# Performance work log

Measured on AMD Instinct MI355X. Metric: run time of the kernel, lower is better.

The kernel has to match this reference:

```python
import jax, jax.numpy as jnp
import numpy as np

EPS = 1e-5  # torch LayerNorm default


def _ln(x, g, b):
    mu = jnp.mean(x, axis=-1, keepdims=True)
    var = jnp.var(x, axis=-1, keepdims=True)
    return (x - mu) * jax.lax.rsqrt(var + EPS) * g + b


def _linear(x, w, b):
    # torch nn.Linear: y = x @ W^T + b, W is [out, in]
    return jnp.einsum('bnc,dc->bnd', x, w) + b


def setup_inputs() -> dict:
    key = jax.random.key(0)
    ks = jax.random.split(key, 12)
    B, C, H, W = 16, 768, 32, 32
    s = 1.0 / np.sqrt(C)
    inp = {
        'x_rgb': jax.random.normal(ks[0], (B, C, H, W), jnp.float32),
        'x_tir': jax.random.normal(ks[1], (B, C, H, W), jnp.float32),
        'x_before': jax.random.normal(ks[2], (B, C, H, W), jnp.float32),
        'w0': jax.random.uniform(ks[3], (C, C), jnp.float32, -s, s),
        'b0': jax.random.uniform(ks[4], (C,), jnp.float32, -s, s),
        'w1': jax.random.uniform(ks[5], (C, C), jnp.float32, -s, s),
        'b1': jax.random.uniform(ks[6], (C,), jnp.float32, -s, s),
        'w2': jax.random.uniform(ks[7], (C, C), jnp.float32, -s, s),
        'b2': jax.random.uniform(ks[8], (C,), jnp.float32, -s, s),
        'ln_g': jnp.ones((C,), jnp.float32),
        'ln_b': jnp.zeros((C,), jnp.float32),
        'wp': jax.random.uniform(ks[9], (C, C), jnp.float32, -s, s),
        'bp': jax.random.uniform(ks[10], (C,), jnp.float32, -s, s),
    }
    return inp


def reference(x_rgb, x_tir, x_before, w0, b0, w1, b1, w2, b2, ln_g, ln_b, wp, bp):
    B, C, H, W = x_rgb.shape
    N = H * W
    scale = C ** (-0.5)
    # flatten(2).permute(0,2,1): [B,C,H,W] -> [B, N, C]
    to_tok = lambda x: jnp.transpose(x.reshape(B, C, N), (0, 2, 1))
    r = _linear(_ln(to_tok(x_rgb), ln_g, ln_b), w0, b0)
    t = _linear(_ln(to_tok(x_tir), ln_g, ln_b), w1, b1)
    f = _linear(_ln(to_tok(x_before), ln_g, ln_b), w2, b2)
    x_sum = r + t
    x_mul = r * t
    # attention: [B, N, N]
    attn = jax.nn.softmax(jnp.einsum('bnc,bmc->bnm', r, f) * scale, axis=-1)
    mid = jnp.einsum('bnm,bmc->bnc', attn, t)
    # faithful to torch: .transpose(1,2).reshape(B, N, C) (element reorder)
    mid = jnp.transpose(mid, (0, 2, 1)).reshape(B, N, C)
    x_middle = x_sum + mid
    x_middle = x_middle + _linear(_ln(x_middle, ln_g, ln_b), wp, bp)
    res = jax.nn.gelu(x_sum, approximate=False) * x_middle \
        + jax.nn.gelu(x_mul, approximate=False) * x_middle
    return res.reshape(B, C, H, W)
```

## Files before the change

### kernel.cpp

```cpp
#include <hip/hip_runtime.h>
#include <hip/hip_bf16.h>
#include <math.h>

typedef unsigned short u16;
typedef __attribute__((ext_vector_type(8))) short bf16x8;
typedef __attribute__((ext_vector_type(4))) float f32x4;
typedef __attribute__((ext_vector_type(4))) u16 u16x4;

#define DEVI static __device__ __forceinline__

DEVI float bf2f(u16 h){ union{unsigned u; float f;} v; v.u=((unsigned)h)<<16; return v.f; }
DEVI u16 f2bf(float x){ union{float f; unsigned u;} v; v.f=x; unsigned r=v.u+0x7fffu+((v.u>>16)&1u); return (u16)(r>>16); }
DEVI void split2(float x, u16 &h, u16 &l){ h=f2bf(x); l=f2bf(x-bf2f(h)); }
DEVI float geluf(float x){ return 0.5f*x*(1.0f+erff(x*0.70710678118654752f)); }

#define GLD16(g,s) __builtin_amdgcn_global_load_lds((const __attribute__((address_space(1))) void*)(g), (__attribute__((address_space(3))) void*)(s), 16, 0, 0)

__global__ void ln_stats_k(const float* __restrict__ x0, const float* __restrict__ x1,
                           const float* __restrict__ x2, float* __restrict__ muS,
                           float* __restrict__ rsS)
{
  const int inp = blockIdx.y;
  const float* x = inp==0?x0:(inp==1?x1:x2);
  const int T0 = blockIdx.x*64;
  const int b = T0>>10, n0 = T0&1023;
  const int tid = threadIdx.x;
  const int n = tid&63, part = tid>>6;
  const float* base = x + ((size_t)b*768)*1024 + n0 + n;
  float s=0.f, s2=0.f;
  for (int c=part;c<768;c+=4){ float v = base[(size_t)c*1024]; s+=v; s2+=v*v; }
  __shared__ float r1[256], r2[256];
  r1[tid]=s; r2[tid]=s2; __syncthreads();
  if (tid<64){
    s = r1[tid]+r1[tid+64]+r1[tid+128]+r1[tid+192];
    s2= r2[tid]+r2[tid+64]+r2[tid+128]+r2[tid+192];
    float mu = s*(1.f/768.f);
    float var = s2*(1.f/768.f)-mu*mu;
    muS[inp*16384+T0+tid]=mu;
    rsS[inp*16384+T0+tid]=rsqrtf(var+1e-5f);
  }
}

__global__ void ln_apply_k(const float* __restrict__ x, const float* __restrict__ muS,
                           const float* __restrict__ rsS, const float* __restrict__ g,
                           const float* __restrict__ be, u16* __restrict__ Ah,
                           u16* __restrict__ Al, int inp)
{
  const int b = blockIdx.y;
  const int gx = blockIdx.x;
  const int c0=(gx%24)*32, n0=(gx/24)*32;
  const int tid=threadIdx.x;
  __shared__ u16 Hh[32][33], Hl[32][33];
  const int nl=tid&31, cp=tid>>5;
  const int tok = b*1024 + n0 + nl;
  const float mu = muS[inp*16384+tok], rs = rsS[inp*16384+tok];
  #pragma unroll
  for (int i=0;i<4;i++){
    int cl = cp + i*8;
    int c = c0 + cl;
    float v = x[((size_t)(b*768+c))*1024 + n0 + nl];
    float y = (v-mu)*rs*g[c]+be[c];
    u16 h,l; split2(y,h,l);
    Hh[cl][nl]=h; Hl[cl][nl]=l;
  }
  __syncthreads();
  const int wn = tid>>3, wc=(tid&7)*4;
  u16x4 vh, vl;
  #pragma unroll
  for (int j=0;j<4;j++){ vh[j]=Hh[wc+j][wn]; vl[j]=Hl[wc+j][wn]; }
  size_t o = ((size_t)(b*1024+n0+wn))*768 + c0 + wc;
  *(u16x4*)(Ah+o)=vh; *(u16x4*)(Al+o)=vl;
}

__global__ void wsplit_k(const float* __restrict__ w0,const float* __restrict__ w1,
                         const float* __restrict__ w2,const float* __restrict__ wpk,
                         u16* __restrict__ wh, u16* __restrict__ wl)
{
  const int ws = blockIdx.y;
  const float* w = ws==0?w0:(ws==1?w1:(ws==2?w2:wpk));
  int i = blockIdx.x*256+threadIdx.x;
  u16 h,l; split2(w[i],h,l);
  wh[(size_t)ws*589824+i]=h; wl[(size_t)ws*589824+i]=l;
}

__global__ void tr_pairs_k(const u16* __restrict__ Sh, const u16* __restrict__ Sl,
                           u16* __restrict__ Dh, u16* __restrict__ Dl)
{
  const int b = blockIdx.y;
  const int gx = blockIdx.x;
  const int c0=(gx%24)*32, n0=(gx/24)*32;
  const int tid=threadIdx.x;
  __shared__ u16 Th[32][33], Tl[32][33];
  const int cl=tid&31, np=tid>>5;
  #pragma unroll
  for (int i=0;i<4;i++){
    int nl = np + i*8;
    size_t o = ((size_t)(b*1024+n0+nl))*768 + c0 + cl;
    Th[cl][nl]=Sh[o]; Tl[cl][nl]=Sl[o];
  }
  __syncthreads();
  const int nl2=tid&31, cp2=tid>>5;
  #pragma unroll
  for (int i=0;i<4;i++){
    int cl2 = cp2 + i*8;
    size_t o = ((size_t)b*786432) + (size_t)(c0+cl2)*1024 + n0 + nl2;
    Dh[o]=Th[cl2][nl2]; Dl[o]=Tl[cl2][nl2];
  }
}

__global__ void softmax_k(float* __restrict__ S)
{
  const long row = blockIdx.x;
  const int tid=threadIdx.x;
  const int lane=tid&63, wid=tid>>6;
  float4 v4 = *(const float4*)(S + row*1024 + tid*4);
  float m = fmaxf(fmaxf(v4.x,v4.y),fmaxf(v4.z,v4.w));
  for (int o=1;o<64;o<<=1) m = fmaxf(m, __shfl_xor(m,o,64));
  __shared__ float red[4]; __shared__ float red2[4];
  if (lane==0) red[wid]=m;
  __syncthreads();
  m = fmaxf(fmaxf(red[0],red[1]),fmaxf(red[2],red[3]));
  float e0=__expf(v4.x-m), e1=__expf(v4.y-m), e2=__expf(v4.z-m), e3=__expf(v4.w-m);
  float s = e0+e1+e2+e3;
  for (int o=1;o<64;o<<=1) s += __shfl_xor(s,o,64);
  if (lane==0) red2[wid]=s;
  __syncthreads();
  s = red2[0]+red2[1]+red2[2]+red2[3];
  float inv = 1.f/s;
  u16x4 h4,l4;
  u16 h,l;
  split2(e0*inv,h,l); h4[0]=h; l4[0]=l;
  split2(e1*inv,h,l); h4[1]=h; l4[1]=l;
  split2(e2*inv,h,l); h4[2]=h; l4[2]=l;
  split2(e3*inv,h,l); h4[3]=h; l4[3]=l;
  u16* base = (u16*)S + row*2048;
  *(u16x4*)(base + tid*4)        = h4;
  *(u16x4*)(base + 1024 + tid*4) = l4;
}

__global__ void midtr_k(const float* __restrict__ mid, const u16* __restrict__ rh,
                        const u16* __restrict__ rl, const u16* __restrict__ th,
                        const u16* __restrict__ tl, float* __restrict__ xm)
{
  const int b=blockIdx.y;
  const int gx=blockIdx.x;
  const int c0=(gx%24)*32, n0=(gx/24)*32;
  const int tid=threadIdx.x;
  __shared__ float T[32][33];
  const int cl=tid&31, np=tid>>5;
  #pragma unroll
  for (int i=0;i<4;i++){
    int nl=np+i*8;
    T[cl][nl] = mid[((size_t)b*786432)+(size_t)(n0+nl)*768 + c0+cl];
  }
  __syncthreads();
  const int nl2=tid&31, cp2=tid>>5;
  #pragma unroll
  for (int i=0;i<4;i++){
    int cl2=cp2+i*8;
    size_t j = (size_t)(c0+cl2)*1024 + n0+nl2;
    size_t gi = (size_t)b*786432 + j;
    float rv = bf2f(rh[gi])+bf2f(rl[gi]);
    float tv = bf2f(th[gi])+bf2f(tl[gi]);
    xm[gi] = rv+tv+T[cl2][nl2];
  }
}

__global__ void ln_rows_k(const float* __restrict__ x, const float* __restrict__ g,
                          const float* __restrict__ be, u16* __restrict__ Oh, u16* __restrict__ Ol)
{
  const long row=blockIdx.x;
  const int tid=threadIdx.x;
  const float* xr = x + row*768;
  float v0=xr[tid], v1=xr[tid+256], v2=xr[tid+512];
  float s=v0+v1+v2, s2=v0*v0+v1*v1+v2*v2;
  for (int o=1;o<64;o<<=1){ s+=__shfl_xor(s,o,64); s2+=__shfl_xor(s2,o,64); }
  __shared__ float rA[4]; __shared__ float rB[4];
  const int lane=tid&63, wid=tid>>6;
  if(lane==0){rA[wid]=s;rB[wid]=s2;}
  __syncthreads();
  s=rA[0]+rA[1]+rA[2]+rA[3]; s2=rB[0]+rB[1]+rB[2]+rB[3];
  float mu=s*(1.f/768.f), var=s2*(1.f/768.f)-mu*mu, rs=rsqrtf(var+1e-5f);
  u16 h,l;
  float y0=(v0-mu)*rs*g[tid]+be[tid];         split2(y0,h,l); Oh[row*768+tid]=h;     Ol[row*768+tid]=l;
  float y1=(v1-mu)*rs*g[tid+256]+be[tid+256]; split2(y1,h,l); Oh[row*768+tid+256]=h; Ol[row*768+tid+256]=l;
  float y2=(v2-mu)*rs*g[tid+512]+be[tid+512]; split2(y2,h,l); Oh[row*768+tid+512]=h; Ol[row*768+tid+512]=l;
}

template<int EPI>
__launch_bounds__(256,2)
__global__ void gemm3_k(const u16* __restrict__ Ah, const u16* __restrict__ Al, long aBat, int lda,
                        const u16* __restrict__ Bh, const u16* __restrict__ Bl, long bBat, int ldb,
                        int K, int tilesM, int ldo, long oBat, float scaleV,
                        const float* __restrict__ bias,
                        u16* __restrict__ Oh, u16* __restrict__ Ol,
                        float* __restrict__ outF,
                        const float* __restrict__ xmid,
                        const u16* __restrict__ rhp, const u16* __restrict__ rlp,
                        const u16* __restrict__ thp, const u16* __restrict__ tlp,
                        float* __restrict__ dout)
{
  __shared__ u16 sm[16384];
  u16* sAh=sm; u16* sAl=sm+4096; u16* sBh=sm+8192; u16* sBl=sm+12288;
  const int tid=threadIdx.x, lane=tid&63, wid=tid>>6;
  const int wm=(wid&1)*64, wn=(wid>>1)*64;
  const int tm = (blockIdx.x % tilesM)*128;
  const int tn = (blockIdx.x / tilesM)*128;
  const int batch = blockIdx.y;
  const u16* gAh = Ah + (long)batch*aBat + (long)tm*lda;
  const u16* gAl = Al + (long)batch*aBat + (long)tm*lda;
  const u16* gBh = Bh + (long)batch*bBat + (long)tn*ldb;
  const u16* gBl = Bl + (long)batch*bBat + (long)tn*ldb;
  f32x4 acc[4][4];
  #pragma unroll
  for(int i=0;i<4;i++)
    #pragma unroll
    for(int j=0;j<4;j++) acc[i][j]=(f32x4){0.f,0.f,0.f,0.f};
  const int frow=lane&15, fko=(lane>>4)<<3;
  const int nkt=K>>5;
  for(int kt=0;kt<nkt;kt++){
    const int k0=kt<<5;
    __syncthreads();
    #pragma unroll
    for(int is=0;is<2;is++){
      int idx=is*256+tid;
      int mm=idx>>2, ko=(idx&3)<<3;
      long goA=(long)mm*lda + k0 + ko;
      long goB=(long)mm*ldb + k0 + ko;
      int so=(idx & ~63)*8;
      GLD16(gAh+goA, sAh+so);
      GLD16(gAl+goA, sAl+so);
      GLD16(gBh+goB, sBh+so);
      GLD16(gBl+goB, sBl+so);
    }
    __syncthreads();
    bf16x8 fbh[4], fbl[4];
    #pragma unroll
    for(int j=0;j<4;j++){
      int off=(wn+j*16+frow)*32+fko;
      fbh[j]=*(const bf16x8*)(sBh+off);
      fbl[j]=*(const bf16x8*)(sBl+off);
    }
    #pragma unroll
    for(int i=0;i<4;i++){
      int off=(wm+i*16+frow)*32+fko;
      bf16x8 fah=*(const bf16x8*)(sAh+off);
      bf16x8 fal=*(const bf16x8*)(sAl+off);
      #pragma unroll
      for(int j=0;j<4;j++){
        acc[i][j]=__builtin_amdgcn_mfma_f32_16x16x32_bf16(fah,fbh[j],acc[i][j],0,0,0);
        acc[i][j]=__builtin_amdgcn_mfma_f32_16x16x32_bf16(fah,fbl[j],acc[i][j],0,0,0);
        acc[i][j]=__builtin_amdgcn_mfma_f32_16x16x32_bf16(fal,fbh[j],acc[i][j],0,0,0);
      }
    }
  }
  const int r0 = tm+wm+((lane>>4)<<2);
  const int c0 = tn+wn+(lane&15);
  #pragma unroll
  for(int i=0;i<4;i++){
    #pragma unroll
    for(int q=0;q<4;q++){
      int r = r0 + i*16 + q;
      #pragma unroll
      for(int j=0;j<4;j++){
        int cc = c0 + j*16;
        float v = acc[i][j][q];
        long o = (long)batch*oBat + (long)(r>>10)*oBat + (long)(r&1023)*ldo + cc;
        if constexpr (EPI==0){
          v += bias[cc];
          u16 h,l; split2(v,h,l);
          Oh[o]=h; Ol[o]=l;
        } else if constexpr (EPI==1){
          outF[o] = v*scaleV;
        } else if constexpr (EPI==2){
          outF[o] = v;
        } else {
          float lin = v + bias[cc];
          float xmv = xmid[o];
          float rv = bf2f(rhp[o])+bf2f(rlp[o]);
          float tv = bf2f(thp[o])+bf2f(tlp[o]);
          float xs=rv+tv, xmu=rv*tv;
          dout[o] = (geluf(xs)+geluf(xmu))*(xmv+lin);
        }
      }
    }
  }
}

extern "C" void kernel_launch(void* const* d_in, const int* in_sizes, int n_in,
                              void* d_out, int out_size, void* d_ws, size_t ws_size,
                              hipStream_t stream)
{
  const float* x_rgb=(const float*)d_in[0];
  const float* x_tir=(const float*)d_in[1];
  const float* x_bef=(const float*)d_in[2];
  const float* w0=(const float*)d_in[3];
  const float* b0=(const float*)d_in[4];
  const float* w1=(const float*)d_in[5];
  const float* b1=(const float*)d_in[6];
  const float* w2=(const float*)d_in[7];
  const float* b2=(const float*)d_in[8];
  const float* lng=(const float*)d_in[9];
  const float* lnb=(const float*)d_in[10];
  const float* wpk=(const float*)d_in[11];
  const float* bp=(const float*)d_in[12];
  float* out=(float*)d_out;

  char* wsb=(char*)d_ws;
  size_t off=0;
  auto alloc=[&](size_t bytes)->char*{ char* p=wsb+off; off=(off+bytes+255)&~(size_t)255; return p; };

  const long PAIRE = (long)16384*768;
  float* muS = (float*)alloc(3*16384*4);
  float* rsS = (float*)alloc(3*16384*4);
  u16* wh = (u16*)alloc(4*589824*2);
  u16* wl = (u16*)alloc(4*589824*2);
  char* stageA = alloc((size_t)2*PAIRE*2);
  u16* sAh=(u16*)stageA;      u16* sAl=sAh+PAIRE;
  u16* tTh=sAh;               u16* tTl=sAh+PAIRE;
  u16* xmh=sAh;               u16* xml=sAh+PAIRE;
  u16* rh=(u16*)alloc(PAIRE*2); u16* rl=(u16*)alloc(PAIRE*2);
  u16* th=(u16*)alloc(PAIRE*2); u16* tl=(u16*)alloc(PAIRE*2);
  char* fmid = alloc((size_t)2*PAIRE*2);
  u16* fb=(u16*)fmid;
  float* midf=(float*)fmid;
  char* SPx = alloc((size_t)2*PAIRE*2);
  float* Sf=(float*)SPx;
  u16* Pu=(u16*)SPx;
  float* xmf=(float*)SPx;

  if (off > ws_size){
    hipMemsetAsync(d_out, 0, (size_t)out_size*4, stream);
    return;
  }

  const float SC = 0.03608439182435161f;
  dim3 blk(256);

  wsplit_k<<<dim3(2304,4),blk,0,stream>>>(w0,w1,w2,wpk,wh,wl);
  ln_stats_k<<<dim3(256,3),blk,0,stream>>>(x_rgb,x_tir,x_bef,muS,rsS);

  ln_apply_k<<<dim3(768,16),blk,0,stream>>>(x_rgb,muS,rsS,lng,lnb,sAh,sAl,0);
  gemm3_k<0><<<dim3(128*6,1),blk,0,stream>>>(sAh,sAl,0,768, wh,wl,0,768, 768,128,768,786432, 0.f,
      b0, rh,rl, nullptr, nullptr,nullptr,nullptr,nullptr,nullptr,nullptr);
  ln_apply_k<<<dim3(768,16),blk,0,stream>>>(x_tir,muS,rsS,lng,lnb,sAh,sAl,1);
  gemm3_k<0><<<dim3(128*6,1),blk,0,stream>>>(sAh,sAl,0,768, wh+589824,wl+589824,0,768, 768,128,768,786432, 0.f,
      b1, th,tl, nullptr, nullptr,nullptr,nullptr,nullptr,nullptr,nullptr);
  ln_apply_k<<<dim3(768,16),blk,0,stream>>>(x_bef,muS,rsS,lng,lnb,sAh,sAl,2);
  gemm3_k<0><<<dim3(128*6,1),blk,0,stream>>>(sAh,sAl,0,768, wh+2*589824,wl+2*589824,0,768, 768,128,768,1572864, 0.f,
      b2, fb,fb+786432, nullptr, nullptr,nullptr,nullptr,nullptr,nullptr,nullptr);

  tr_pairs_k<<<dim3(768,16),blk,0,stream>>>(th,tl,tTh,tTl);

  for (int c=0;c<2;c++){
    long cb = (long)c*8;
    gemm3_k<1><<<dim3(8*8,8),blk,0,stream>>>(rh+cb*786432,rl+cb*786432,786432,768,
        fb+cb*1572864,fb+786432+cb*1572864,1572864,768,
        768,8,1024,1048576, SC, nullptr, nullptr,nullptr, Sf,
        nullptr,nullptr,nullptr,nullptr,nullptr,nullptr);
    softmax_k<<<dim3(8192),blk,0,stream>>>(Sf);
    gemm3_k<2><<<dim3(8*6,8),blk,0,stream>>>(Pu,Pu+1024,2097152,2048,
        tTh+cb*786432,tTl+cb*786432,786432,1024,
        1024,8,768,786432, 0.f, nullptr, nullptr,nullptr, midf+cb*786432,
        nullptr,nullptr,nullptr,nullptr,nullptr,nullptr);
  }

  midtr_k<<<dim3(768,16),blk,0,stream>>>(midf,rh,rl,th,tl,xmf);
  ln_rows_k<<<dim3(16384),blk,0,stream>>>(xmf,lng,lnb,xmh,xml);
  gemm3_k<3><<<dim3(128*6,1),blk,0,stream>>>(xmh,xml,0,768, wh+3*589824,wl+3*589824,0,768,
      768,128,768,786432, 0.f, bp, nullptr,nullptr, nullptr, xmf, rh,rl,th,tl, out);
}
```

Baseline: 921.3 us.

## Fuse mid transpose and residual add into PV GEMM epilogue; split LN stats

Adds an EPI==4 epilogue to the attention-times-T GEMM that writes its result transposed and adds r+t directly into x_middle, which removes the separate midtr_k transpose kernel and its extra round trip through global memory. LayerNorm statistics are now computed with a two-stage reduction: a partial-sum kernel with more blocks and float4 loads over channel chunks, then a finalize kernel. This raises parallelism for the stats pass. The transposed stores in the fused epilogue are strided across columns, which may coalesce poorly, and workspace layout changes so midf is reused as x_middle.

```diff
diff --git a/kernel.cpp b/kernel.cpp
--- a/kernel.cpp
+++ b/kernel.cpp
@@ -16,29 +16,45 @@
 
 #define GLD16(g,s) __builtin_amdgcn_global_load_lds((const __attribute__((address_space(1))) void*)(g), (__attribute__((address_space(3))) void*)(s), 16, 0, 0)
 
-__global__ void ln_stats_k(const float* __restrict__ x0, const float* __restrict__ x1,
-                           const float* __restrict__ x2, float* __restrict__ muS,
-                           float* __restrict__ rsS)
+__global__ void ln_part_k(const float* __restrict__ x0, const float* __restrict__ x1,
+                          const float* __restrict__ x2, float* __restrict__ sP,
+                          float* __restrict__ s2P)
 {
   const int inp = blockIdx.y;
   const float* x = inp==0?x0:(inp==1?x1:x2);
-  const int T0 = blockIdx.x*64;
+  const int tile = blockIdx.x>>3, chunk = blockIdx.x&7;
+  const int T0 = tile*256;
   const int b = T0>>10, n0 = T0&1023;
-  const int tid = threadIdx.x;
-  const int n = tid&63, part = tid>>6;
-  const float* base = x + ((size_t)b*768)*1024 + n0 + n;
+  const int tid = threadIdx.x, lane = tid&63, part = tid>>6;
+  const float* base = x + ((size_t)b*768 + chunk*96)*1024 + n0 + lane*4;
+  float4 s = {0,0,0,0}, s2 = {0,0,0,0};
+  for (int c=part; c<96; c+=4){
+    float4 v = *(const float4*)(base + (size_t)c*1024);
+    s.x+=v.x; s.y+=v.y; s.z+=v.z; s.w+=v.w;
+    s2.x+=v.x*v.x; s2.y+=v.y*v.y; s2.z+=v.z*v.z; s2.w+=v.w*v.w;
+  }
+  __shared__ float4 L1[4][64], L2[4][64];
+  L1[part][lane]=s; L2[part][lane]=s2;
+  __syncthreads();
+  const float* f1=(const float*)L1; const float* f2=(const float*)L2;
+  float a  = f1[tid]+f1[256+tid]+f1[512+tid]+f1[768+tid];
+  float a2 = f2[tid]+f2[256+tid]+f2[512+tid]+f2[768+tid];
+  long o = (long)inp*131072 + (long)chunk*16384 + T0 + tid;
+  sP[o]=a; s2P[o]=a2;
+}
+
+__global__ void ln_fin_k(const float* __restrict__ sP, const float* __restrict__ s2P,
+                         float* __restrict__ muS, float* __restrict__ rsS)
+{
+  int i = blockIdx.x*256+threadIdx.x;
+  int inp = i>>14, ti = i&16383;
+  long base = (long)inp*131072 + ti;
   float s=0.f, s2=0.f;
-  for (int c=part;c<768;c+=4){ float v = base[(size_t)c*1024]; s+=v; s2+=v*v; }
-  __shared__ float r1[256], r2[256];
-  r1[tid]=s; r2[tid]=s2; __syncthreads();
-  if (tid<64){
-    s = r1[tid]+r1[tid+64]+r1[tid+128]+r1[tid+192];
-    s2= r2[tid]+r2[tid+64]+r2[tid+128]+r2[tid+192];
-    float mu = s*(1.f/768.f);
-    float var = s2*(1.f/768.f)-mu*mu;
-    muS[inp*16384+T0+tid]=mu;
-    rsS[inp*16384+T0+tid]=rsqrtf(var+1e-5f);
-  }
+  #pragma unroll
+  for (int k=0;k<8;k++){ s += sP[base+(long)k*16384]; s2 += s2P[base+(long)k*16384]; }
+  float mu = s*(1.f/768.f);
+  float var = s2*(1.f/768.f)-mu*mu;
+  muS[i]=mu; rsS[i]=rsqrtf(var+1e-5f);
 }
 
 __global__ void ln_apply_k(const float* __restrict__ x, const float* __restrict__ muS,
@@ -136,34 +152,6 @@
   u16* base = (u16*)S + row*2048;
   *(u16x4*)(base + tid*4)        = h4;
   *(u16x4*)(base + 1024 + tid*4) = l4;
-}
-
-__global__ void midtr_k(const float* __restrict__ mid, const u16* __restrict__ rh,
-                        const u16* __restrict__ rl, const u16* __restrict__ th,
-                        const u16* __restrict__ tl, float* __restrict__ xm)
-{
-  const int b=blockIdx.y;
-  const int gx=blockIdx.x;
-  const int c0=(gx%24)*32, n0=(gx/24)*32;
-  const int tid=threadIdx.x;
-  __shared__ float T[32][33];
-  const int cl=tid&31, np=tid>>5;
-  #pragma unroll
-  for (int i=0;i<4;i++){
-    int nl=np+i*8;
-    T[cl][nl] = mid[((size_t)b*786432)+(size_t)(n0+nl)*768 + c0+cl];
-  }
-  __syncthreads();
-  const int nl2=tid&31, cp2=tid>>5;
-  #pragma unroll
-  for (int i=0;i<4;i++){
-    int cl2=cp2+i*8;
-    size_t j = (size_t)(c0+cl2)*1024 + n0+nl2;
-    size_t gi = (size_t)b*786432 + j;
-    float rv = bf2f(rh[gi])+bf2f(rl[gi]);
-    float tv = bf2f(th[gi])+bf2f(tl[gi]);
-    xm[gi] = rv+tv+T[cl2][nl2];
-  }
 }
 
 __global__ void ln_rows_k(const float* __restrict__ x, const float* __restrict__ g,
@@ -265,22 +253,29 @@
       for(int j=0;j<4;j++){
         int cc = c0 + j*16;
         float v = acc[i][j][q];
-        long o = (long)batch*oBat + (long)(r>>10)*oBat + (long)(r&1023)*ldo + cc;
-        if constexpr (EPI==0){
-          v += bias[cc];
-          u16 h,l; split2(v,h,l);
-          Oh[o]=h; Ol[o]=l;
-        } else if constexpr (EPI==1){
-          outF[o] = v*scaleV;
-        } else if constexpr (EPI==2){
-          outF[o] = v;
+        if constexpr (EPI==4){
+          long o2 = (long)batch*oBat + (long)cc*1024 + (r&1023);
+          float rv = bf2f(rhp[o2])+bf2f(rlp[o2]);
+          float tv = bf2f(thp[o2])+bf2f(tlp[o2]);
+          outF[o2] = (rv+tv)+v;
         } else {
-          float lin = v + bias[cc];
-          float xmv = xmid[o];
-          float rv = bf2f(rhp[o])+bf2f(rlp[o]);
-          float tv = bf2f(thp[o])+bf2f(tlp[o]);
-          float xs=rv+tv, xmu=rv*tv;
-          dout[o] = (geluf(xs)+geluf(xmu))*(xmv+lin);
+          long o = (long)batch*oBat + (long)(r>>10)*oBat + (long)(r&1023)*ldo + cc;
+          if constexpr (EPI==0){
+            v += bias[cc];
+            u16 h,l; split2(v,h,l);
+            Oh[o]=h; Ol[o]=l;
+          } else if constexpr (EPI==1){
+            outF[o] = v*scaleV;
+          } else if constexpr (EPI==2){
+            outF[o] = v;
+          } else {
+            float lin = v + bias[cc];
+            float xmv = xmid[o];
+            float rv = bf2f(rhp[o])+bf2f(rlp[o]);
+            float tv = bf2f(thp[o])+bf2f(tlp[o]);
+            float xs=rv+tv, xmu=rv*tv;
+            dout[o] = (geluf(xs)+geluf(xmu))*(xmv+lin);
+          }
         }
       }
     }
@@ -313,6 +308,8 @@
   const long PAIRE = (long)16384*768;
   float* muS = (float*)alloc(3*16384*4);
   float* rsS = (float*)alloc(3*16384*4);
+  float* sP  = (float*)alloc((size_t)3*8*16384*4);
+  float* s2P = (float*)alloc((size_t)3*8*16384*4);
   u16* wh = (u16*)alloc(4*589824*2);
   u16* wl = (u16*)alloc(4*589824*2);
   char* stageA = alloc((size_t)2*PAIRE*2);
@@ -324,10 +321,9 @@
   char* fmid = alloc((size_t)2*PAIRE*2);
   u16* fb=(u16*)fmid;
   float* midf=(float*)fmid;
-  char* SPx = alloc((size_t)2*PAIRE*2);
+  char* SPx = alloc((size_t)8*1024*1024*4);
   float* Sf=(float*)SPx;
   u16* Pu=(u16*)SPx;
-  float* xmf=(float*)SPx;
 
   if (off > ws_size){
     hipMemsetAsync(d_out, 0, (size_t)out_size*4, stream);
@@ -338,7 +334,8 @@
   dim3 blk(256);
 
   wsplit_k<<<dim3(2304,4),blk,0,stream>>>(w0,w1,w2,wpk,wh,wl);
-  ln_stats_k<<<dim3(256,3),blk,0,stream>>>(x_rgb,x_tir,x_bef,muS,rsS);
+  ln_part_k<<<dim3(512,3),blk,0,stream>>>(x_rgb,x_tir,x_bef,sP,s2P);
+  ln_fin_k<<<dim3(192),blk,0,stream>>>(sP,s2P,muS,rsS);
 
   ln_apply_k<<<dim3(768,16),blk,0,stream>>>(x_rgb,muS,rsS,lng,lnb,sAh,sAl,0);
   gemm3_k<0><<<dim3(128*6,1),blk,0,stream>>>(sAh,sAl,0,768, wh,wl,0,768, 768,128,768,786432, 0.f,
@@ -359,14 +356,13 @@
         768,8,1024,1048576, SC, nullptr, nullptr,nullptr, Sf,
         nullptr,nullptr,nullptr,nullptr,nullptr,nullptr);
     softmax_k<<<dim3(8192),blk,0,stream>>>(Sf);
-    gemm3_k<2><<<dim3(8*6,8),blk,0,stream>>>(Pu,Pu+1024,2097152,2048,
+    gemm3_k<4><<<dim3(8*6,8),blk,0,stream>>>(Pu,Pu+1024,2097152,2048,
         tTh+cb*786432,tTl+cb*786432,786432,1024,
-        1024,8,768,786432, 0.f, nullptr, nullptr,nullptr, midf+cb*786432,
-        nullptr,nullptr,nullptr,nullptr,nullptr,nullptr);
-  }
-
-  midtr_k<<<dim3(768,16),blk,0,stream>>>(midf,rh,rl,th,tl,xmf);
-  ln_rows_k<<<dim3(16384),blk,0,stream>>>(xmf,lng,lnb,xmh,xml);
+        1024,8,1024,786432, 0.f, nullptr, nullptr,nullptr, midf+cb*786432,
+        nullptr, rh+cb*786432,rl+cb*786432, th+cb*786432,tl+cb*786432, nullptr);
+  }
+
+  ln_rows_k<<<dim3(16384),blk,0,stream>>>(midf,lng,lnb,xmh,xml);
   gemm3_k<3><<<dim3(128*6,1),blk,0,stream>>>(xmh,xml,0,768, wh+3*589824,wl+3*589824,0,768,
-      768,128,768,786432, 0.f, bp, nullptr,nullptr, nullptr, xmf, rh,rl,th,tl, out);
-}
+      768,128,768,786432, 0.f, bp, nullptr,nullptr, nullptr, midf, rh,rl,th,tl, out);
+}
```

Result: faster. 892.5 us (-3.1%).
